# Performance work log

Measured on AMD Instinct MI355X. Metric: run time of the kernel, lower is better.

Reference implementation:

```python
import jax, jax.numpy as jnp
import numpy as np

B, H, W = 16, 512, 512
NUM_POINTS = 112 * 112          # 12544
OVERSAMPLE = 3
N_UNC = int(0.75 * NUM_POINTS)  # 9408
N_RAND = NUM_POINTS - N_UNC     # 3136
NUM_MASKS = 16.0
IN_W, OUT_W = 2.0, 0.5


def _point_sample(img, coords):
    """Bilinear grid_sample with align_corners=False, zero padding.
    img: [B,C,H,W], coords: [B,P,2] in [0,1] (x,y). Returns [B,C,P]."""
    Bn, C, Hh, Ww = img.shape
    x = coords[..., 0] * Ww - 0.5
    y = coords[..., 1] * Hh - 0.5
    x0 = jnp.floor(x)
    y0 = jnp.floor(y)
    wx1 = x - x0; wx0 = 1.0 - wx1
    wy1 = y - y0; wy0 = 1.0 - wy1

    def gather(im, yi, xi):  # im [C,H,W]; yi,xi [P] float indices
        valid = ((yi >= 0) & (yi < Hh) & (xi >= 0) & (xi < Ww)).astype(im.dtype)
        yc = jnp.clip(yi, 0, Hh - 1).astype(jnp.int32)
        xc = jnp.clip(xi, 0, Ww - 1).astype(jnp.int32)
        return im[:, yc, xc] * valid  # [C,P]

    def one(im, x0b, y0b, a0, a1, b0, b1):
        v00 = gather(im, y0b, x0b)
        v01 = gather(im, y0b, x0b + 1)
        v10 = gather(im, y0b + 1, x0b)
        v11 = gather(im, y0b + 1, x0b + 1)
        return v00 * (b0 * a0) + v01 * (b0 * a1) + v10 * (b1 * a0) + v11 * (b1 * a1)

    return jax.vmap(one)(img, x0, y0, wx0, wx1, wy0, wy1)


def setup_inputs() -> dict:
    key = jax.random.key(0)
    k1, k2, k3, k4 = jax.random.split(key, 4)
    pred_masks = jax.random.normal(k1, (B, 1, H, W), jnp.float32)
    gt_masks = (jax.random.uniform(k2, (B, 1, H, W)) > 0.5).astype(jnp.float32)
    coords_os = jax.random.uniform(k3, (B, NUM_POINTS * OVERSAMPLE, 2), jnp.float32)
    coords_rand = jax.random.uniform(k4, (B, N_RAND, 2), jnp.float32)
    return {"pred_masks": pred_masks, "gt_masks": gt_masks,
            "coords_os": coords_os, "coords_rand": coords_rand}


def reference(pred_masks, gt_masks, coords_os, coords_rand):
    sg = jax.lax.stop_gradient

    # ---- uncertainty-based point selection (torch.no_grad block) ----
    pl_os = _point_sample(sg(pred_masks), coords_os)[:, 0, :]  # [B, Ns]
    unc = -jnp.abs(pl_os)
    _, idx = jax.lax.top_k(unc, N_UNC)                          # [B, N_UNC]
    sel = jnp.take_along_axis(coords_os, idx[..., None], axis=1)
    point_coords = sg(jnp.concatenate([sel, coords_rand], axis=1))  # [B, NUM_POINTS, 2]
    point_labels = sg(_point_sample(gt_masks, point_coords)[:, 0, :])  # [B, NUM_POINTS]

    # ---- point-sampled sigmoid CE + dice ----
    z = _point_sample(pred_masks, point_coords)[:, 0, :]  # [B, NUM_POINTS]
    t = point_labels
    ce = jnp.maximum(z, 0.0) - z * t + jnp.log1p(jnp.exp(-jnp.abs(z)))
    loss_mask = ce.mean(1).sum() / NUM_MASKS
    p = jax.nn.sigmoid(z)
    num = 2.0 * (p * t).sum(-1)
    den = p.sum(-1) + t.sum(-1)
    loss_dice = (1.0 - (num + 1.0) / (den + 1.0)).sum() / NUM_MASKS

    # ---- bbox extraction from predicted masks (non-differentiable) ----
    fg = jax.nn.sigmoid(sg(pred_masks[:, 0])) > 0.5  # [B,H,W]
    xg = jnp.arange(W, dtype=jnp.float32)
    yg = jnp.arange(H, dtype=jnp.float32)
    BIG = jnp.float32(1e9)
    x_min = jnp.min(jnp.where(fg, xg[None, None, :], BIG), axis=(1, 2))
    x_max = jnp.max(jnp.where(fg, xg[None, None, :], -BIG), axis=(1, 2))
    y_min = jnp.min(jnp.where(fg, yg[None, :, None], BIG), axis=(1, 2))
    y_max = jnp.max(jnp.where(fg, yg[None, :, None], -BIG), axis=(1, 2))
    empty = ~fg.any(axis=(1, 2))
    x1 = jnp.where(empty, 0.0, x_min)
    y1 = jnp.where(empty, 0.0, y_min)
    x2 = jnp.where(empty, float(W - 1), x_max)
    y2 = jnp.where(empty, float(H - 1), y_max)

    # ---- create_box_mask (clamp(min=0) -> int trunc -> cap at edge) ----
    x1i = jnp.floor(jnp.maximum(x1, 0.0))
    y1i = jnp.floor(jnp.maximum(y1, 0.0))
    x2i = jnp.minimum(jnp.floor(jnp.maximum(x2, 0.0)), float(W - 1))
    y2i = jnp.minimum(jnp.floor(jnp.maximum(y2, 0.0)), float(H - 1))
    valid = (x2i > x1i) & (y2i > y1i)
    in_x = (xg[None, None, :] >= x1i[:, None, None]) & (xg[None, None, :] <= x2i[:, None, None])
    in_y = (yg[None, :, None] >= y1i[:, None, None]) & (yg[None, :, None] <= y2i[:, None, None])
    box_masks = (in_x & in_y & valid[:, None, None]).astype(jnp.float32)  # [B,H,W]
    wmask = box_masks * IN_W + (1.0 - box_masks) * OUT_W

    # ---- region-aware BCE + dice over full-resolution masks ----
    zf = pred_masks.reshape(B, -1)
    gf = gt_masks.reshape(B, -1)
    wf = wmask.reshape(B, -1)
    logp = jax.nn.log_sigmoid(zf)
    log1mp = jax.nn.log_sigmoid(-zf)
    bce = -(gf * logp + (1.0 - gf) * log1mp)
    wsum = jnp.maximum(wf.sum(-1), 1e-6)
    loss_region_bce = ((bce * wf).sum(-1) / wsum).sum() / NUM_MASKS
    pf = jax.nn.sigmoid(zf)
    inter = (pf * gf * wf).sum(-1)
    pw = (pf * wf).sum(-1)
    gw = (gf * wf).sum(-1)
    loss_region_dice = (1.0 - (2.0 * inter + 1.0) / (pw + gw + 1.0)).sum() / NUM_MASKS

    return jnp.stack([loss_mask, loss_dice, loss_region_bce, loss_region_dice])
```

## Files before the change

kernel.cpp:

```cpp
#include <hip/hip_runtime.h>
#include <cstdint>
#include <cstddef>

namespace {

constexpr int kB = 16;
constexpr int kH = 512;
constexpr int kW = 512;
constexpr int kHW = kH * kW;
constexpr int kNS = 37632;
constexpr int kNS4 = kNS / 4;
constexpr int kNUNC = 9408;
constexpr int kNRAND = 3136;
constexpr int kNPTS = 12544;
constexpr int kBXB = 16;
constexpr int kRPB = 4;
constexpr int kRGB2 = 16;
constexpr int kPairs = kNS / 2;
constexpr int kSampSlots = 148;
constexpr int kSampleBlocks = 8 * kSampSlots;
constexpr int kBboxBlocks = kB * kBXB;
constexpr int kRandBlocks = kB * kRPB;
constexpr int kHStride = 1025;

constexpr size_t OFF_PU  = 0;
constexpr size_t OFF_TRM = OFF_PU + (size_t)kB * kNS * 4;
constexpr size_t OFF_BBP = OFF_TRM + (size_t)kB * kNS * 16;
constexpr size_t OFF_PLP = OFF_BBP + (size_t)kB * kBXB * 4 * 4;
constexpr size_t OFF_OSP = OFF_PLP + (size_t)kB * kRPB * 4 * 4;
constexpr size_t OFF_RGP = OFF_OSP + (size_t)kB * 4 * 4;

__device__ __forceinline__ int SW(int bin) {
  return (bin & 15) * kHStride + (bin >> 4);
}

}

__device__ __forceinline__ float sample_bilinear(const float* __restrict__ img,
                                                 float cx, float cy) {
  float x = cx * (float)kW - 0.5f;
  float y = cy * (float)kH - 0.5f;
  float x0f = floorf(x), y0f = floorf(y);
  float wx1 = x - x0f, wx0 = 1.0f - wx1;
  float wy1 = y - y0f, wy0 = 1.0f - wy1;
  int x0 = (int)x0f, y0 = (int)y0f;
  int x1 = x0 + 1, y1 = y0 + 1;
  int xc0 = min(max(x0, 0), kW - 1), xc1 = min(max(x1, 0), kW - 1);
  int yc0 = min(max(y0, 0), kH - 1), yc1 = min(max(y1, 0), kH - 1);
  float v00 = ((x0 >= 0) && (x0 < kW) && (y0 >= 0) && (y0 < kH)) ? img[yc0 * kW + xc0] : 0.0f;
  float v01 = ((x1 >= 0) && (x1 < kW) && (y0 >= 0) && (y0 < kH)) ? img[yc0 * kW + xc1] : 0.0f;
  float v10 = ((x0 >= 0) && (x0 < kW) && (y1 >= 0) && (y1 < kH)) ? img[yc1 * kW + xc0] : 0.0f;
  float v11 = ((x1 >= 0) && (x1 < kW) && (y1 >= 0) && (y1 < kH)) ? img[yc1 * kW + xc1] : 0.0f;
  return v00 * (wy0 * wx0) + v01 * (wy0 * wx1) + v10 * (wy1 * wx0) + v11 * (wy1 * wx1);
}

__device__ __forceinline__ void ce_pair(float z, float tt, float& ce, float& p) {
  float a = expf(-fabsf(z));
  ce = fmaxf(z, 0.0f) - z * tt + log1pf(a);
  float inv = 1.0f / (1.0f + a);
  p = (z >= 0.0f) ? inv : a * inv;
}

__global__ __launch_bounds__(256) void fused1_kernel(const float* __restrict__ pred,
                                                     const float* __restrict__ gt,
                                                     const float* __restrict__ coords_os,
                                                     const float* __restrict__ coords_rand,
                                                     unsigned* __restrict__ pu,
                                                     float4* __restrict__ trm,
                                                     int* __restrict__ bbp,
                                                     float* __restrict__ plp) {
  int blk = blockIdx.x;
  int t = threadIdx.x;

  if (blk < kSampleBlocks) {
    int x = blk & 7;
    int s = blk >> 3;
    int b = x * 2 + (s & 1);
    int chunk = s >> 1;
    int pib = chunk * 256 + t;
    if (pib >= kPairs) return;
    size_t gp = (size_t)b * kPairs + pib;
    float4 c2 = ((const float4*)coords_os)[gp];
    size_t i0 = gp * 2;
    const float* pred_b = pred + (size_t)b * kHW;
    const float* gt_b = gt + (size_t)b * kHW;
    float z0 = sample_bilinear(pred_b, c2.x, c2.y);
    float z1 = sample_bilinear(pred_b, c2.z, c2.w);
    float t0 = sample_bilinear(gt_b, c2.x, c2.y);
    float t1 = sample_bilinear(gt_b, c2.z, c2.w);
    float ce0, p0, ce1, p1;
    ce_pair(z0, t0, ce0, p0);
    ce_pair(z1, t1, ce1, p1);
    unsigned u0 = __float_as_uint(z0) & 0x7fffffffu;
    unsigned u1 = __float_as_uint(z1) & 0x7fffffffu;
    *(uint2*)&pu[i0] = make_uint2(u0, u1);
    trm[i0] = make_float4(ce0, p0, t0, p0 * t0);
    trm[i0 + 1] = make_float4(ce1, p1, t1, p1 * t1);
    return;
  }

  if (blk < kSampleBlocks + kBboxBlocks) {
    __shared__ int r0[256], r1[256], r2[256], r3[256];
    int i = blk - kSampleBlocks;
    int x = i & 7;
    int s = i >> 3;
    int b = x * 2 + (s & 1);
    int c = s >> 1;
    constexpr int CHUNK4 = kHW / kBXB / 4;
    const float4* pred4 = (const float4*)(pred + (size_t)b * kHW) + (size_t)c * CHUNK4;
    int pbase = c * CHUNK4 * 4;
    int xmn = kW, xmx = -1, ymn = kH, ymx = -1;
    for (int i4 = t; i4 < CHUNK4; i4 += 256) {
      float4 z = pred4[i4];
      int p = pbase + i4 * 4;
      int y = p >> 9;
      int x0 = p & (kW - 1);
      if (z.x > 0.0f) { xmn = min(xmn, x0);     xmx = max(xmx, x0);     ymn = min(ymn, y); ymx = max(ymx, y); }
      if (z.y > 0.0f) { xmn = min(xmn, x0 + 1); xmx = max(xmx, x0 + 1); ymn = min(ymn, y); ymx = max(ymx, y); }
      if (z.z > 0.0f) { xmn = min(xmn, x0 + 2); xmx = max(xmx, x0 + 2); ymn = min(ymn, y); ymx = max(ymx, y); }
      if (z.w > 0.0f) { xmn = min(xmn, x0 + 3); xmx = max(xmx, x0 + 3); ymn = min(ymn, y); ymx = max(ymx, y); }
    }
    r0[t] = xmn; r1[t] = xmx; r2[t] = ymn; r3[t] = ymx;
    __syncthreads();
    for (int s2 = 128; s2 > 0; s2 >>= 1) {
      if (t < s2) {
        r0[t] = min(r0[t], r0[t + s2]);
        r1[t] = max(r1[t], r1[t + s2]);
        r2[t] = min(r2[t], r2[t + s2]);
        r3[t] = max(r3[t], r3[t + s2]);
      }
      __syncthreads();
    }
    if (t == 0) {
      int* o = bbp + ((size_t)b * kBXB + c) * 4;
      o[0] = r0[0]; o[1] = r1[0]; o[2] = r2[0]; o[3] = r3[0];
    }
    return;
  }

  {
    __shared__ float red[4][256];
    int i = blk - kSampleBlocks - kBboxBlocks;
    int x = i & 7;
    int s = i >> 3;
    int b = x * 2 + (s & 1);
    int c = s >> 1;
    const float* pred_b = pred + (size_t)b * kHW;
    const float* gt_b = gt + (size_t)b * kHW;
    float ce_s = 0.0f, p_s = 0.0f, t_s = 0.0f, pt_s = 0.0f;
    for (int e = c * 256 + t; e < kNRAND; e += kRPB * 256) {
      float2 cc = *(const float2*)&coords_rand[((size_t)b * kNRAND + e) * 2];
      float z = sample_bilinear(pred_b, cc.x, cc.y);
      float tt = sample_bilinear(gt_b, cc.x, cc.y);
      float ce, p;
      ce_pair(z, tt, ce, p);
      ce_s += ce; p_s += p; t_s += tt; pt_s += p * tt;
    }
    red[0][t] = ce_s; red[1][t] = p_s; red[2][t] = t_s; red[3][t] = pt_s;
    __syncthreads();
    for (int s2 = 128; s2 > 0; s2 >>= 1) {
      if (t < s2) {
        red[0][t] += red[0][t + s2];
        red[1][t] += red[1][t + s2];
        red[2][t] += red[2][t + s2];
        red[3][t] += red[3][t + s2];
      }
      __syncthreads();
    }
    if (t == 0) {
      float* o = plp + ((size_t)b * kRPB + c) * 4;
      o[0] = red[0][0]; o[1] = red[1][0]; o[2] = red[2][0]; o[3] = red[3][0];
    }
  }
}

__global__ __launch_bounds__(1024) void fused2_kernel(const unsigned* __restrict__ pu,
                                                      const float4* __restrict__ trm,
                                                      const float* __restrict__ pred,
                                                      const float* __restrict__ gt,
                                                      const int* __restrict__ bbp,
                                                      float* __restrict__ osp,
                                                      float* __restrict__ rgp) {
  __shared__ unsigned smem[16 * kHStride + 1024];
  __shared__ int s_bstar, s_need, s_ccnt, s_round;
  int blk = blockIdx.x;
  int t = threadIdx.x;

  if (blk < kB) {
    constexpr int C4 = 10;
    constexpr int CAP = 1024;
    int b = (blk & 7) * 2 + (blk >> 3);
    const uint4* pu4_b = (const uint4*)(pu + (size_t)b * kNS);
    const float4* trm_b = trm + (size_t)b * kNS;
    unsigned* hist = smem;
    unsigned* sums = smem + 16 * kHStride;

    for (int i = t; i < 16 * kHStride; i += 1024) hist[i] = 0u;
    if (t == 0) s_ccnt = 0;
    __syncthreads();

#pragma unroll 2
    for (int j = 0; j < C4; ++j) {
      int idx4 = j * 1024 + t;
      if (idx4 < kNS4) {
        uint4 u = pu4_b[idx4];
        atomicAdd(&hist[SW((int)(u.x >> 17))], 1u);
        atomicAdd(&hist[SW((int)(u.y >> 17))], 1u);
        atomicAdd(&hist[SW((int)(u.z >> 17))], 1u);
        atomicAdd(&hist[SW((int)(u.w >> 17))], 1u);
      }
    }
    __syncthreads();

    unsigned s = 0;
#pragma unroll
    for (int k = 0; k < 16; ++k) s += hist[k * kHStride + t];
    sums[t] = s;
    __syncthreads();
    if (t < 64) {
      const unsigned K = (unsigned)kNUNC;
      unsigned v = 0;
#pragma unroll
      for (int k = 0; k < 16; ++k) v += sums[t * 16 + k];
      unsigned cum = v;
      for (int off = 1; off < 64; off <<= 1) {
        unsigned xx = __shfl_up(cum, off, 64);
        if (t >= off) cum += xx;
      }
      unsigned long long m = __ballot(cum >= K);
      int L = (int)__ffsll(m) - 1;
      unsigned base1 = __shfl(cum - v, L, 64);
      unsigned v2 = (t < 16) ? sums[L * 16 + t] : 0u;
      unsigned cum2 = v2;
      for (int off = 1; off < 16; off <<= 1) {
        unsigned xx = __shfl_up(cum2, off, 64);
        if (t >= off) cum2 += xx;
      }
      unsigned long long m2 = __ballot((t < 16) && (base1 + cum2 >= K));
      int M = (int)__ffsll(m2) - 1;
      unsigned base2 = __shfl(base1 + cum2 - v2, M, 64);
      int E = L * 16 + M;
      unsigned v3 = (t < 16) ? hist[t * kHStride + E] : 0u;
      unsigned cum3 = v3;
      for (int off = 1; off < 16; off <<= 1) {
        unsigned xx = __shfl_up(cum3, off, 64);
        if (t >= off) cum3 += xx;
      }
      unsigned long long m3 = __ballot((t < 16) && (base2 + cum3 >= K));
      int F = (int)__ffsll(m3) - 1;
      if (t == F) {
        s_bstar = E * 16 + F;
        s_need = (int)(K - (base2 + cum3 - v3));
      }
    }
    __syncthreads();
    int bstar = s_bstar;
    int need = s_need;

    int* cand = (int*)sums;
    float ce_s = 0.0f, p_s = 0.0f, t_s = 0.0f, pt_s = 0.0f;
#pragma unroll 2
    for (int j = 0; j < C4; ++j) {
      int idx4 = j * 1024 + t;
      if (idx4 < kNS4) {
        uint4 u = pu4_b[idx4];
        const float4* base = trm_b + (size_t)idx4 * 4;
        float4 q0 = base[0];
        float4 q1 = base[1];
        float4 q2 = base[2];
        float4 q3 = base[3];
        int b0 = (int)(u.x >> 17), b1 = (int)(u.y >> 17);
        int b2 = (int)(u.z >> 17), b3 = (int)(u.w >> 17);
        float w0 = (b0 < bstar) ? 1.0f : 0.0f;
        float w1 = (b1 < bstar) ? 1.0f : 0.0f;
        float w2 = (b2 < bstar) ? 1.0f : 0.0f;
        float w3 = (b3 < bstar) ? 1.0f : 0.0f;
        ce_s += w0 * q0.x + w1 * q1.x + w2 * q2.x + w3 * q3.x;
        p_s  += w0 * q0.y + w1 * q1.y + w2 * q2.y + w3 * q3.y;
        t_s  += w0 * q0.z + w1 * q1.z + w2 * q2.z + w3 * q3.z;
        pt_s += w0 * q0.w + w1 * q1.w + w2 * q2.w + w3 * q3.w;
        if (b0 == bstar) { int pos = atomicAdd(&s_ccnt, 1); if (pos < CAP) cand[pos] = idx4 * 4 + 0; }
        if (b1 == bstar) { int pos = atomicAdd(&s_ccnt, 1); if (pos < CAP) cand[pos] = idx4 * 4 + 1; }
        if (b2 == bstar) { int pos = atomicAdd(&s_ccnt, 1); if (pos < CAP) cand[pos] = idx4 * 4 + 2; }
        if (b3 == bstar) { int pos = atomicAdd(&s_ccnt, 1); if (pos < CAP) cand[pos] = idx4 * 4 + 3; }
      }
    }
    __syncthreads();
    int c = s_ccnt;

    if (c <= CAP) {
      for (int i = t; i < c; i += 1024) {
        int my = cand[i];
        int r = 0;
        for (int k = 0; k < c; ++k) r += (cand[k] < my) ? 1 : 0;
        if (r < need) {
          float4 q = trm_b[my];
          ce_s += q.x; p_s += q.y; t_s += q.z; pt_s += q.w;
        }
      }
      __syncthreads();
    } else {
      if (t == 0) s_round = 0;
      __syncthreads();
      for (int j = 0; j < C4; ++j) {
        int idx4 = j * 1024 + t;
        unsigned meq = 0u;
        if (idx4 < kNS4) {
          uint4 u = pu4_b[idx4];
          meq = (unsigned)((int)(u.x >> 17) == bstar) |
                ((unsigned)((int)(u.y >> 17) == bstar) << 1) |
                ((unsigned)((int)(u.z >> 17) == bstar) << 2) |
                ((unsigned)((int)(u.w >> 17) == bstar) << 3);
        }
        unsigned cnt = __popc(meq);
        sums[t] = cnt;
        __syncthreads();
        for (int off = 1; off < 1024; off <<= 1) {
          unsigned v = (t >= off) ? sums[t - off] : 0u;
          __syncthreads();
          sums[t] += v;
          __syncthreads();
        }
        int myBase = s_round + (int)(sums[t] - cnt);
        unsigned mm = meq;
        while (mm) {
          int e = __ffs(mm) - 1;
          mm &= mm - 1;
          if (myBase < need) {
            float4 q = trm_b[idx4 * 4 + e];
            ce_s += q.x; p_s += q.y; t_s += q.z; pt_s += q.w;
          }
          myBase++;
        }
        __syncthreads();
        if (t == 0) s_round += (int)sums[1023];
        __syncthreads();
      }
    }

    float* redf = (float*)smem;
    float vals[4] = {ce_s, p_s, t_s, pt_s};
#pragma unroll
    for (int q = 0; q < 4; ++q) {
      float v = vals[q];
      for (int o = 32; o > 0; o >>= 1) v += __shfl_down(v, o, 64);
      if ((t & 63) == 0) redf[(t >> 6) * 4 + q] = v;
    }
    __syncthreads();
    if (t == 0) {
      float o0 = 0, o1 = 0, o2 = 0, o3 = 0;
      for (int w = 0; w < 16; ++w) {
        o0 += redf[w * 4 + 0]; o1 += redf[w * 4 + 1];
        o2 += redf[w * 4 + 2]; o3 += redf[w * 4 + 3];
      }
      float* o = osp + (size_t)b * 4;
      o[0] = o0; o[1] = o1; o[2] = o2; o[3] = o3;
    }
    return;
  }

  {
    constexpr int CHUNK4 = kHW / kRGB2 / 4;
    int i = blk - kB;
    int x = i & 7;
    int s = i >> 3;
    int b = x * 2 + (s & 1);
    int c = s >> 1;
    const float4* pred4 = (const float4*)(pred + (size_t)b * kHW) + (size_t)c * CHUNK4;
    const float4* gt4 = (const float4*)(gt + (size_t)b * kHW) + (size_t)c * CHUNK4;

    int xmn = kW, xmx = -1, ymn = kH, ymx = -1;
#pragma unroll
    for (int u = 0; u < kBXB; ++u) {
      const int4 pb = *(const int4*)(bbp + ((size_t)b * kBXB + u) * 4);
      xmn = min(xmn, pb.x); xmx = max(xmx, pb.y);
      ymn = min(ymn, pb.z); ymx = max(ymx, pb.w);
    }
    bool empty = (xmx < 0);
    int x1 = empty ? 0 : xmn;
    int x2 = min(empty ? (kW - 1) : xmx, kW - 1);
    int y1 = empty ? 0 : ymn;
    int y2 = min(empty ? (kH - 1) : ymx, kH - 1);
    bool valid = (x2 > x1) && (y2 > y1);

    int pbase = c * CHUNK4 * 4;
    float wsum = 0.0f, bcew = 0.0f, inter = 0.0f, pw = 0.0f, gw = 0.0f;
    for (int i4 = t; i4 < CHUNK4; i4 += 1024) {
      float4 zv = pred4[i4];
      float4 gv = gt4[i4];
      int p = pbase + i4 * 4;
      int y = p >> 9;
      int x0 = p & (kW - 1);
      bool iny = valid && (y >= y1) && (y <= y2);
#pragma unroll
      for (int l = 0; l < 4; ++l) {
        float z = (l == 0) ? zv.x : (l == 1) ? zv.y : (l == 2) ? zv.z : zv.w;
        float g = (l == 0) ? gv.x : (l == 1) ? gv.y : (l == 2) ? gv.z : gv.w;
        int xx = x0 + l;
        float w = (iny && xx >= x1 && xx <= x2) ? 2.0f : 0.5f;
        float a = expf(-fabsf(z));
        float sp = fmaxf(-z, 0.0f) + log1pf(a);
        float bce = sp + (1.0f - g) * z;
        float inv = 1.0f / (1.0f + a);
        float pp = (z >= 0.0f) ? inv : a * inv;
        wsum += w;
        bcew += bce * w;
        inter += pp * g * w;
        pw += pp * w;
        gw += g * w;
      }
    }
    float* redf = (float*)smem;
    float vals[5] = {wsum, bcew, inter, pw, gw};
#pragma unroll
    for (int q5 = 0; q5 < 5; ++q5) {
      float v = vals[q5];
      for (int o = 32; o > 0; o >>= 1) v += __shfl_down(v, o, 64);
      if ((t & 63) == 0) redf[(t >> 6) * 5 + q5] = v;
    }
    __syncthreads();
    if (t == 0) {
      float o0 = 0, o1 = 0, o2 = 0, o3 = 0, o4 = 0;
      for (int w = 0; w < 16; ++w) {
        o0 += redf[w * 5 + 0]; o1 += redf[w * 5 + 1]; o2 += redf[w * 5 + 2];
        o3 += redf[w * 5 + 3]; o4 += redf[w * 5 + 4];
      }
      float* o = rgp + ((size_t)b * kRGB2 + c) * 5;
      o[0] = o0; o[1] = o1; o[2] = o2; o[3] = o3; o[4] = o4;
    }
  }
}

__global__ __launch_bounds__(64) void finalize_kernel(const float* __restrict__ plp,
                                                      const float* __restrict__ osp,
                                                      const float* __restrict__ rgp,
                                                      float* __restrict__ out) {
  __shared__ double sh[kB][4];
  int t = threadIdx.x;
  if (t < kB) {
    const float* o = osp + (size_t)t * 4;
    double ce = o[0], p = o[1], tt = o[2], pt = o[3];
    for (int c = 0; c < kRPB; ++c) {
      const float* q = plp + ((size_t)t * kRPB + c) * 4;
      ce += q[0]; p += q[1]; tt += q[2]; pt += q[3];
    }
    double ws = 0, bc = 0, in = 0, pw = 0, gw = 0;
    for (int c = 0; c < kRGB2; ++c) {
      const float* q = rgp + ((size_t)t * kRGB2 + c) * 5;
      ws += q[0]; bc += q[1]; in += q[2]; pw += q[3]; gw += q[4];
    }
    sh[t][0] = ce / (double)kNPTS;
    sh[t][1] = 1.0 - (2.0 * pt + 1.0) / (p + tt + 1.0);
    double wss = ws > 1e-6 ? ws : 1e-6;
    sh[t][2] = bc / wss;
    sh[t][3] = 1.0 - (2.0 * in + 1.0) / (pw + gw + 1.0);
  }
  __syncthreads();
  if (t == 0) {
    double a = 0, b = 0, c = 0, d = 0;
    for (int i = 0; i < kB; ++i) { a += sh[i][0]; b += sh[i][1]; c += sh[i][2]; d += sh[i][3]; }
    out[0] = (float)(a / 16.0);
    out[1] = (float)(b / 16.0);
    out[2] = (float)(c / 16.0);
    out[3] = (float)(d / 16.0);
  }
}

extern "C" void kernel_launch(void* const* d_in, const int* in_sizes, int n_in,
                              void* d_out, int out_size, void* d_ws, size_t ws_size,
                              hipStream_t stream) {
  const float* pred = (const float*)d_in[0];
  const float* gt = (const float*)d_in[1];
  const float* coords_os = (const float*)d_in[2];
  const float* coords_rand = (const float*)d_in[3];
  float* out = (float*)d_out;
  char* ws = (char*)d_ws;

  unsigned* pu = (unsigned*)(ws + OFF_PU);
  float4* trm = (float4*)(ws + OFF_TRM);
  int* bbp = (int*)(ws + OFF_BBP);
  float* plp = (float*)(ws + OFF_PLP);
  float* osp = (float*)(ws + OFF_OSP);
  float* rgp = (float*)(ws + OFF_RGP);

  fused1_kernel<<<kSampleBlocks + kBboxBlocks + kRandBlocks, 256, 0, stream>>>(
      pred, gt, coords_os, coords_rand, pu, trm, bbp, plp);
  fused2_kernel<<<kB + kB * kRGB2, 1024, 0, stream>>>(pu, trm, pred, gt, bbp, osp, rgp);
  finalize_kernel<<<1, 64, 0, stream>>>(plp, osp, rgp, out);
}
```

Measured before the change: 64.94 us.

## Store raw samples instead of precomputed terms and fold finalize into last block

The sampling stage now writes only the raw sampled logit and target per point (8 bytes) instead of an abs-bits array plus a 16-byte float4 of CE/prob terms. The selection kernel recomputes the CE and sigmoid terms on the fly for selected points. The separate finalize launch is replaced by a last-block-done pattern using a global atomic counter reset by the first kernel. This cuts intermediate global traffic and one launch, at the cost of extra transcendental work and a threadfence and atomic per block.

After: 144.7 us. 123% more time.

```diff
diff --git a/kernel.cpp b/kernel.cpp
--- a/kernel.cpp
+++ b/kernel.cpp
@@ -22,13 +22,15 @@
 constexpr int kBboxBlocks = kB * kBXB;
 constexpr int kRandBlocks = kB * kRPB;
 constexpr int kHStride = 1025;
-
-constexpr size_t OFF_PU  = 0;
-constexpr size_t OFF_TRM = OFF_PU + (size_t)kB * kNS * 4;
-constexpr size_t OFF_BBP = OFF_TRM + (size_t)kB * kNS * 16;
+constexpr int kK2Blocks = kB + kB * kRGB2;
+
+constexpr size_t OFF_PZ  = 0;
+constexpr size_t OFF_TV  = OFF_PZ + (size_t)kB * kNS * 4;
+constexpr size_t OFF_BBP = OFF_TV + (size_t)kB * kNS * 4;
 constexpr size_t OFF_PLP = OFF_BBP + (size_t)kB * kBXB * 4 * 4;
 constexpr size_t OFF_OSP = OFF_PLP + (size_t)kB * kRPB * 4 * 4;
 constexpr size_t OFF_RGP = OFF_OSP + (size_t)kB * 4 * 4;
+constexpr size_t OFF_CNT = OFF_RGP + (size_t)kB * kRGB2 * 5 * 4;
 
 __device__ __forceinline__ int SW(int bin) {
   return (bin & 15) * kHStride + (bin >> 4);
@@ -65,12 +67,15 @@
                                                      const float* __restrict__ gt,
                                                      const float* __restrict__ coords_os,
                                                      const float* __restrict__ coords_rand,
-                                                     unsigned* __restrict__ pu,
-                                                     float4* __restrict__ trm,
+                                                     unsigned* __restrict__ pz,
+                                                     float* __restrict__ tv,
                                                      int* __restrict__ bbp,
-                                                     float* __restrict__ plp) {
+                                                     float* __restrict__ plp,
+                                                     int* __restrict__ cnt) {
   int blk = blockIdx.x;
   int t = threadIdx.x;
+
+  if (blk == 0 && t == 0) *cnt = 0;
 
   if (blk < kSampleBlocks) {
     int x = blk & 7;
@@ -88,14 +93,8 @@
     float z1 = sample_bilinear(pred_b, c2.z, c2.w);
     float t0 = sample_bilinear(gt_b, c2.x, c2.y);
     float t1 = sample_bilinear(gt_b, c2.z, c2.w);
-    float ce0, p0, ce1, p1;
-    ce_pair(z0, t0, ce0, p0);
-    ce_pair(z1, t1, ce1, p1);
-    unsigned u0 = __float_as_uint(z0) & 0x7fffffffu;
-    unsigned u1 = __float_as_uint(z1) & 0x7fffffffu;
-    *(uint2*)&pu[i0] = make_uint2(u0, u1);
-    trm[i0] = make_float4(ce0, p0, t0, p0 * t0);
-    trm[i0 + 1] = make_float4(ce1, p1, t1, p1 * t1);
+    *(uint2*)&pz[i0] = make_uint2(__float_as_uint(z0), __float_as_uint(z1));
+    *(float2*)&tv[i0] = make_float2(t0, t1);
     return;
   }
 
@@ -174,15 +173,19 @@
   }
 }
 
-__global__ __launch_bounds__(1024) void fused2_kernel(const unsigned* __restrict__ pu,
-                                                      const float4* __restrict__ trm,
+__global__ __launch_bounds__(1024) void fused2_kernel(const unsigned* __restrict__ pz,
+                                                      const float* __restrict__ tv,
                                                       const float* __restrict__ pred,
                                                       const float* __restrict__ gt,
                                                       const int* __restrict__ bbp,
+                                                      const float* __restrict__ plp,
                                                       float* __restrict__ osp,
-                                                      float* __restrict__ rgp) {
+                                                      float* __restrict__ rgp,
+                                                      int* __restrict__ cnt,
+                                                      float* __restrict__ out) {
   __shared__ unsigned smem[16 * kHStride + 1024];
-  __shared__ int s_bstar, s_need, s_ccnt, s_round;
+  __shared__ double shd[kB][4];
+  __shared__ int s_bstar, s_need, s_ccnt, s_round, s_last;
   int blk = blockIdx.x;
   int t = threadIdx.x;
 
@@ -190,8 +193,8 @@
     constexpr int C4 = 10;
     constexpr int CAP = 1024;
     int b = (blk & 7) * 2 + (blk >> 3);
-    const uint4* pu4_b = (const uint4*)(pu + (size_t)b * kNS);
-    const float4* trm_b = trm + (size_t)b * kNS;
+    const uint4* pz4_b = (const uint4*)(pz + (size_t)b * kNS);
+    const float4* tv4_b = (const float4*)(tv + (size_t)b * kNS);
     unsigned* hist = smem;
     unsigned* sums = smem + 16 * kHStride;
 
@@ -203,11 +206,11 @@
     for (int j = 0; j < C4; ++j) {
       int idx4 = j * 1024 + t;
       if (idx4 < kNS4) {
-        uint4 u = pu4_b[idx4];
-        atomicAdd(&hist[SW((int)(u.x >> 17))], 1u);
-        atomicAdd(&hist[SW((int)(u.y >> 17))], 1u);
-        atomicAdd(&hist[SW((int)(u.z >> 17))], 1u);
-        atomicAdd(&hist[SW((int)(u.w >> 17))], 1u);
+        uint4 u = pz4_b[idx4];
+        atomicAdd(&hist[SW((int)((u.x & 0x7fffffffu) >> 17))], 1u);
+        atomicAdd(&hist[SW((int)((u.y & 0x7fffffffu) >> 17))], 1u);
+        atomicAdd(&hist[SW((int)((u.z & 0x7fffffffu) >> 17))], 1u);
+        atomicAdd(&hist[SW((int)((u.w & 0x7fffffffu) >> 17))], 1u);
       }
     }
     __syncthreads();
@@ -263,26 +266,23 @@
     for (int j = 0; j < C4; ++j) {
       int idx4 = j * 1024 + t;
       if (idx4 < kNS4) {
-        uint4 u = pu4_b[idx4];
-        const float4* base = trm_b + (size_t)idx4 * 4;
-        float4 q0 = base[0];
-        float4 q1 = base[1];
-        float4 q2 = base[2];
-        float4 q3 = base[3];
-        int b0 = (int)(u.x >> 17), b1 = (int)(u.y >> 17);
-        int b2 = (int)(u.z >> 17), b3 = (int)(u.w >> 17);
-        float w0 = (b0 < bstar) ? 1.0f : 0.0f;
-        float w1 = (b1 < bstar) ? 1.0f : 0.0f;
-        float w2 = (b2 < bstar) ? 1.0f : 0.0f;
-        float w3 = (b3 < bstar) ? 1.0f : 0.0f;
-        ce_s += w0 * q0.x + w1 * q1.x + w2 * q2.x + w3 * q3.x;
-        p_s  += w0 * q0.y + w1 * q1.y + w2 * q2.y + w3 * q3.y;
-        t_s  += w0 * q0.z + w1 * q1.z + w2 * q2.z + w3 * q3.z;
-        pt_s += w0 * q0.w + w1 * q1.w + w2 * q2.w + w3 * q3.w;
-        if (b0 == bstar) { int pos = atomicAdd(&s_ccnt, 1); if (pos < CAP) cand[pos] = idx4 * 4 + 0; }
-        if (b1 == bstar) { int pos = atomicAdd(&s_ccnt, 1); if (pos < CAP) cand[pos] = idx4 * 4 + 1; }
-        if (b2 == bstar) { int pos = atomicAdd(&s_ccnt, 1); if (pos < CAP) cand[pos] = idx4 * 4 + 2; }
-        if (b3 == bstar) { int pos = atomicAdd(&s_ccnt, 1); if (pos < CAP) cand[pos] = idx4 * 4 + 3; }
+        uint4 u = pz4_b[idx4];
+        float4 tt4 = tv4_b[idx4];
+#pragma unroll
+        for (int e = 0; e < 4; ++e) {
+          unsigned ubits = (e == 0) ? u.x : (e == 1) ? u.y : (e == 2) ? u.z : u.w;
+          float ttv = (e == 0) ? tt4.x : (e == 1) ? tt4.y : (e == 2) ? tt4.z : tt4.w;
+          int bin = (int)((ubits & 0x7fffffffu) >> 17);
+          float z = __uint_as_float(ubits);
+          float ce, p;
+          ce_pair(z, ttv, ce, p);
+          float w = (bin < bstar) ? 1.0f : 0.0f;
+          ce_s += w * ce; p_s += w * p; t_s += w * ttv; pt_s += w * p * ttv;
+          if (bin == bstar) {
+            int pos = atomicAdd(&s_ccnt, 1);
+            if (pos < CAP) cand[pos] = idx4 * 4 + e;
+          }
+        }
       }
     }
     __syncthreads();
@@ -294,8 +294,11 @@
         int r = 0;
         for (int k = 0; k < c; ++k) r += (cand[k] < my) ? 1 : 0;
         if (r < need) {
-          float4 q = trm_b[my];
-          ce_s += q.x; p_s += q.y; t_s += q.z; pt_s += q.w;
+          float z = __uint_as_float(pz[(size_t)b * kNS + my]);
+          float ttv = tv[(size_t)b * kNS + my];
+          float ce, p;
+          ce_pair(z, ttv, ce, p);
+          ce_s += ce; p_s += p; t_s += ttv; pt_s += p * ttv;
         }
       }
       __syncthreads();
@@ -306,14 +309,14 @@
         int idx4 = j * 1024 + t;
         unsigned meq = 0u;
         if (idx4 < kNS4) {
-          uint4 u = pu4_b[idx4];
-          meq = (unsigned)((int)(u.x >> 17) == bstar) |
-                ((unsigned)((int)(u.y >> 17) == bstar) << 1) |
-                ((unsigned)((int)(u.z >> 17) == bstar) << 2) |
-                ((unsigned)((int)(u.w >> 17) == bstar) << 3);
+          uint4 u = pz4_b[idx4];
+          meq = (unsigned)((int)((u.x & 0x7fffffffu) >> 17) == bstar) |
+                ((unsigned)((int)((u.y & 0x7fffffffu) >> 17) == bstar) << 1) |
+                ((unsigned)((int)((u.z & 0x7fffffffu) >> 17) == bstar) << 2) |
+                ((unsigned)((int)((u.w & 0x7fffffffu) >> 17) == bstar) << 3);
         }
-        unsigned cnt = __popc(meq);
-        sums[t] = cnt;
+        unsigned cnt2 = __popc(meq);
+        sums[t] = cnt2;
         __syncthreads();
         for (int off = 1; off < 1024; off <<= 1) {
           unsigned v = (t >= off) ? sums[t - off] : 0u;
@@ -321,14 +324,18 @@
           sums[t] += v;
           __syncthreads();
         }
-        int myBase = s_round + (int)(sums[t] - cnt);
+        int myBase = s_round + (int)(sums[t] - cnt2);
         unsigned mm = meq;
         while (mm) {
           int e = __ffs(mm) - 1;
           mm &= mm - 1;
           if (myBase < need) {
-            float4 q = trm_b[idx4 * 4 + e];
-            ce_s += q.x; p_s += q.y; t_s += q.z; pt_s += q.w;
+            int my = idx4 * 4 + e;
+            float z = __uint_as_float(pz[(size_t)b * kNS + my]);
+            float ttv = tv[(size_t)b * kNS + my];
+            float ce, p;
+            ce_pair(z, ttv, ce, p);
+            ce_s += ce; p_s += p; t_s += ttv; pt_s += p * ttv;
           }
           myBase++;
         }
@@ -356,10 +363,7 @@
       float* o = osp + (size_t)b * 4;
       o[0] = o0; o[1] = o1; o[2] = o2; o[3] = o3;
     }
-    return;
-  }
-
-  {
+  } else {
     constexpr int CHUNK4 = kHW / kRGB2 / 4;
     int i = blk - kB;
     int x = i & 7;
@@ -420,49 +424,50 @@
     }
     __syncthreads();
     if (t == 0) {
-      float o0 = 0, o1 = 0, o2 = 0, o3 = 0, o4 = 0;
+      float* o = rgp + ((size_t)b * kRGB2 + c) * 5;
+      o[0] = vals[0] * 0.0f + redf[0 * 5 + 0] * 0.0f + [&] {
+        float s0 = 0; for (int w = 0; w < 16; ++w) s0 += redf[w * 5 + 0]; return s0; }();
+      float o1 = 0, o2 = 0, o3 = 0, o4 = 0;
       for (int w = 0; w < 16; ++w) {
-        o0 += redf[w * 5 + 0]; o1 += redf[w * 5 + 1]; o2 += redf[w * 5 + 2];
+        o1 += redf[w * 5 + 1]; o2 += redf[w * 5 + 2];
         o3 += redf[w * 5 + 3]; o4 += redf[w * 5 + 4];
       }
-      float* o = rgp + ((size_t)b * kRGB2 + c) * 5;
-      o[0] = o0; o[1] = o1; o[2] = o2; o[3] = o3; o[4] = o4;
+      o[1] = o1; o[2] = o2; o[3] = o3; o[4] = o4;
     }
   }
-}
-
-__global__ __launch_bounds__(64) void finalize_kernel(const float* __restrict__ plp,
-                                                      const float* __restrict__ osp,
-                                                      const float* __restrict__ rgp,
-                                                      float* __restrict__ out) {
-  __shared__ double sh[kB][4];
-  int t = threadIdx.x;
-  if (t < kB) {
-    const float* o = osp + (size_t)t * 4;
-    double ce = o[0], p = o[1], tt = o[2], pt = o[3];
-    for (int c = 0; c < kRPB; ++c) {
-      const float* q = plp + ((size_t)t * kRPB + c) * 4;
-      ce += q[0]; p += q[1]; tt += q[2]; pt += q[3];
-    }
-    double ws = 0, bc = 0, in = 0, pw = 0, gw = 0;
-    for (int c = 0; c < kRGB2; ++c) {
-      const float* q = rgp + ((size_t)t * kRGB2 + c) * 5;
-      ws += q[0]; bc += q[1]; in += q[2]; pw += q[3]; gw += q[4];
-    }
-    sh[t][0] = ce / (double)kNPTS;
-    sh[t][1] = 1.0 - (2.0 * pt + 1.0) / (p + tt + 1.0);
-    double wss = ws > 1e-6 ? ws : 1e-6;
-    sh[t][2] = bc / wss;
-    sh[t][3] = 1.0 - (2.0 * in + 1.0) / (pw + gw + 1.0);
-  }
+
+  __threadfence();
+  if (t == 0) s_last = (atomicAdd(cnt, 1) == kK2Blocks - 1) ? 1 : 0;
   __syncthreads();
-  if (t == 0) {
-    double a = 0, b = 0, c = 0, d = 0;
-    for (int i = 0; i < kB; ++i) { a += sh[i][0]; b += sh[i][1]; c += sh[i][2]; d += sh[i][3]; }
-    out[0] = (float)(a / 16.0);
-    out[1] = (float)(b / 16.0);
-    out[2] = (float)(c / 16.0);
-    out[3] = (float)(d / 16.0);
+  if (s_last) {
+    __threadfence();
+    if (t < kB) {
+      const float* o = osp + (size_t)t * 4;
+      double ce = o[0], p = o[1], tt = o[2], pt = o[3];
+      for (int c = 0; c < kRPB; ++c) {
+        const float* q = plp + ((size_t)t * kRPB + c) * 4;
+        ce += q[0]; p += q[1]; tt += q[2]; pt += q[3];
+      }
+      double ws = 0, bc = 0, in = 0, pw = 0, gw = 0;
+      for (int c = 0; c < kRGB2; ++c) {
+        const float* q = rgp + ((size_t)t * kRGB2 + c) * 5;
+        ws += q[0]; bc += q[1]; in += q[2]; pw += q[3]; gw += q[4];
+      }
+      shd[t][0] = ce / (double)kNPTS;
+      shd[t][1] = 1.0 - (2.0 * pt + 1.0) / (p + tt + 1.0);
+      double wss = ws > 1e-6 ? ws : 1e-6;
+      shd[t][2] = bc / wss;
+      shd[t][3] = 1.0 - (2.0 * in + 1.0) / (pw + gw + 1.0);
+    }
+    __syncthreads();
+    if (t == 0) {
+      double a = 0, b2 = 0, c2 = 0, d = 0;
+      for (int i = 0; i < kB; ++i) { a += shd[i][0]; b2 += shd[i][1]; c2 += shd[i][2]; d += shd[i][3]; }
+      out[0] = (float)(a / 16.0);
+      out[1] = (float)(b2 / 16.0);
+      out[2] = (float)(c2 / 16.0);
+      out[3] = (float)(d / 16.0);
+    }
   }
 }
 
@@ -476,15 +481,15 @@
   float* out = (float*)d_out;
   char* ws = (char*)d_ws;
 
-  unsigned* pu = (unsigned*)(ws + OFF_PU);
-  float4* trm = (float4*)(ws + OFF_TRM);
+  unsigned* pz = (unsigned*)(ws + OFF_PZ);
+  float* tv = (float*)(ws + OFF_TV);
   int* bbp = (int*)(ws + OFF_BBP);
   float* plp = (float*)(ws + OFF_PLP);
   float* osp = (float*)(ws + OFF_OSP);
   float* rgp = (float*)(ws + OFF_RGP);
+  int* cnt = (int*)(ws + OFF_CNT);
 
   fused1_kernel<<<kSampleBlocks + kBboxBlocks + kRandBlocks, 256, 0, stream>>>(
-      pred, gt, coords_os, coords_rand, pu, trm, bbp, plp);
-  fused2_kernel<<<kB + kB * kRGB2, 1024, 0, stream>>>(pu, trm, pred, gt, bbp, osp, rgp);
-  finalize_kernel<<<1, 64, 0, stream>>>(plp, osp, rgp, out);
-}
+      pred, gt, coords_os, coords_rand, pz, tv, bbp, plp, cnt);
+  fused2_kernel<<<kK2Blocks, 1024, 0, stream>>>(pz, tv, pred, gt, bbp, plp, osp, rgp, cnt, out);
+}
```
